# Kernel tuning notes

Measured on AMD Instinct MI355X. Metric: run time of the kernel, lower is better.

## Reference

```python
import jax, jax.numpy as jnp
import numpy as np

TEMP = 0.07
BASE_TEMP = 0.07
LOSS_WEIGHT = 0.5
BN_EPS = 1e-5


def _embed(x, w1, b1, gamma, beta, w2, b2):
    # 1x1 conv C->C  (x: [N,C,H,W], w1: [C_out,C_in])
    h = jnp.einsum('nchw,oc->nohw', x, w1) + b1[None, :, None, None]
    # BatchNorm2d in training mode: batch stats over (N,H,W), biased variance
    mean = h.mean(axis=(0, 2, 3), keepdims=True)
    var = h.var(axis=(0, 2, 3), keepdims=True)
    h = (h - mean) * jax.lax.rsqrt(var + BN_EPS)
    h = h * gamma[None, :, None, None] + beta[None, :, None, None]
    h = jax.nn.relu(h)
    h = jnp.einsum('nchw,oc->nohw', h, w2) + b2[None, :, None, None]
    # F.normalize(p=2, dim=1) with eps=1e-12
    nrm = jnp.sqrt(jnp.sum(h * h, axis=1, keepdims=True))
    return h / jnp.maximum(nrm, 1e-12)


def _contrastive(feats_, labels_):
    # feats_: [T, n_view, C]; labels_: [T]
    T, n_view, C = feats_.shape
    mask_small = (labels_[:, None] == labels_[None, :]).astype(feats_.dtype)  # [T,T]
    # torch.cat(torch.unbind(feats_, dim=1), dim=0): view-major ordering
    cf = feats_.transpose(1, 0, 2).reshape(T * n_view, C)
    logits = (cf @ cf.T) / TEMP                                   # [M,M], M=T*n_view
    logits = logits - jax.lax.stop_gradient(jnp.max(logits, axis=1, keepdims=True))
    mask = jnp.tile(mask_small, (n_view, n_view))                  # repeat(anchor_count, contrast_count)
    neg_mask = 1.0 - mask                                          # computed BEFORE diagonal removal
    M = T * n_view
    logits_mask = 1.0 - jnp.eye(M, dtype=feats_.dtype)
    mask = mask * logits_mask
    exp_logits = jnp.exp(logits)
    neg_logits = jnp.sum(exp_logits * neg_mask, axis=1, keepdims=True)
    log_prob = logits - jnp.log(exp_logits + neg_logits)
    mean_log_prob_pos = jnp.sum(mask * log_prob, axis=1) / (jnp.sum(mask, axis=1) + 1e-6)
    loss = -(TEMP / BASE_TEMP) * mean_log_prob_pos
    return jnp.mean(loss)


def setup_inputs() -> dict:
    N, C_in, H, W = 8, 512, 128, 128
    feat_dim, num_classes = 256, 19
    max_views, max_samples, ignore_label = 100, 1024, -1
    rng = np.random.RandomState(0)

    preds_S = rng.randn(N, C_in, H, W).astype(np.float32)
    # gt label map already at (H,W) => nearest interpolation is identity
    gt = rng.randint(0, num_classes, (N, H * W))
    logits_S = rng.randn(N, num_classes, H * W).astype(np.float32)
    predict = logits_S.argmax(axis=1)  # [N, H*W]

    # ---- replicate _hard_anchor_sampling on host (fixed seed) ----
    classes, total = [], 0
    for i in range(N):
        cl = [int(c) for c in np.unique(gt[i])
              if c != ignore_label and (gt[i] == c).sum() > max_views]
        classes.append(cl)
        total += len(cl)
    n_view = min(max_samples // total, max_views)

    b_idx, p_idx, y_cls = [], [], []
    for i in range(N):
        for c in classes[i]:
            hard = np.where((predict[i] == c) & (gt[i] != c))[0]
            easy = np.where((predict[i] == c) & (gt[i] == c))[0]
            nh, ne = len(hard), len(easy)
            if nh >= n_view / 2 and ne >= n_view / 2:
                kh = n_view // 2; ke = n_view - kh
            elif nh >= n_view / 2:
                ke = ne; kh = n_view - ke
            else:
                kh = nh; ke = n_view - kh
            hs = hard[rng.permutation(nh)[:kh]]
            es = easy[rng.permutation(ne)[:ke]]
            b_idx.append(i)
            p_idx.append(np.concatenate([hs, es]))
            y_cls.append(c)

    batch_idx = jnp.asarray(np.array(b_idx), dtype=jnp.int32)          # [T]
    pix_idx = jnp.asarray(np.stack(p_idx), dtype=jnp.int32)            # [T, n_view]
    y_cls = jnp.asarray(np.array(y_cls), dtype=jnp.int32)              # [T]

    def p(shape, scale, k):
        r = np.random.RandomState(k)
        return jnp.asarray((r.randn(*shape) * scale).astype(np.float32))

    return {
        'preds_S': jnp.asarray(preds_S),
        'w1': p((C_in, C_in), 0.02, 1),
        'b1': jnp.zeros((C_in,), jnp.float32),
        'gamma': jnp.ones((C_in,), jnp.float32),
        'beta': jnp.zeros((C_in,), jnp.float32),
        'w2': p((feat_dim, C_in), 0.02, 2),
        'b2': jnp.zeros((feat_dim,), jnp.float32),
        'batch_idx': batch_idx,
        'pix_idx': pix_idx,
        'y_cls': y_cls,
    }


def reference(preds_S, w1, b1, gamma, beta, w2, b2, batch_idx, pix_idx, y_cls):
    f = _embed(preds_S, w1, b1, gamma, beta, w2, b2)        # [N, C, H, W]
    N, C, H, W = f.shape
    feats = f.transpose(0, 2, 3, 1).reshape(N, H * W, C)     # [N, HW, C]
    X_ = feats[batch_idx[:, None], pix_idx]                   # [T, n_view, C]
    labels_ = y_cls.astype(f.dtype)
    return LOSS_WEIGHT * _contrastive(X_, labels_)
```

## Files before the change

### kernel.cpp

```cpp
#include <hip/hip_runtime.h>
#include <hip/hip_bf16.h>

#define C_IN   512
#define C_OUT  256
#define HW     16384
#define NIMG   8
#define PTOT   (NIMG * HW)
#define MP     1024
#define TEMP_INV (1.0f / 0.07f)
#define BN_EPS   1e-5f
#define SPB    4
#define OGRP   8
#define IGRP   8
#define BK     64

typedef float  f32x4  __attribute__((ext_vector_type(4)));
typedef short  short8 __attribute__((ext_vector_type(8)));
typedef short  short4v __attribute__((ext_vector_type(4)));

#define WS_S1   0
#define WS_G    (WS_S1 + C_IN)
#define WS_W1P  (WS_G + C_IN * C_IN)
#define WS_B1P  (WS_W1P + C_IN * C_IN)
#define WS_CF   (WS_B1P + C_IN)
#define WS_XB_F (WS_CF + MP * C_OUT)
#define WS_NEED_FAST ((size_t)WS_XB_F * 4 + (size_t)PTOT * C_IN * 2)

__global__ __launch_bounds__(256)
void kprep(const float* __restrict__ x, __hip_bfloat16* __restrict__ xb,
           float* __restrict__ s1) {
    int plane = blockIdx.x;
    int c = plane & (C_IN - 1);
    const float4* p = (const float4*)(x + (size_t)plane * HW);
    short4v* q = (short4v*)(xb + (size_t)plane * HW);
    float acc = 0.f;
    for (int i = threadIdx.x; i < HW / 4; i += 256) {
        float4 v = p[i];
        acc += v.x + v.y + v.z + v.w;
        union { short4v s; __hip_bfloat162 h[2]; } u;
        u.h[0] = __float22bfloat162_rn(make_float2(v.x, v.y));
        u.h[1] = __float22bfloat162_rn(make_float2(v.z, v.w));
        q[i] = u.s;
    }
    for (int off = 32; off; off >>= 1) acc += __shfl_down(acc, off, 64);
    __shared__ float red[4];
    int lane = threadIdx.x & 63, wv = threadIdx.x >> 6;
    if (lane == 0) red[wv] = acc;
    __syncthreads();
    if (threadIdx.x == 0)
        atomicAdd(&s1[c], red[0] + red[1] + red[2] + red[3]);
}

__global__ __launch_bounds__(256)
void ksum(const float* __restrict__ x, float* __restrict__ s1) {
    int plane = blockIdx.x;
    int c = plane & (C_IN - 1);
    const float4* p = (const float4*)(x + (size_t)plane * HW);
    float acc = 0.f;
    for (int i = threadIdx.x; i < HW / 4; i += 256) {
        float4 v = p[i];
        acc += v.x + v.y + v.z + v.w;
    }
    for (int off = 32; off; off >>= 1) acc += __shfl_down(acc, off, 64);
    __shared__ float red[4];
    int lane = threadIdx.x & 63, wv = threadIdx.x >> 6;
    if (lane == 0) red[wv] = acc;
    __syncthreads();
    if (threadIdx.x == 0)
        atomicAdd(&s1[c], red[0] + red[1] + red[2] + red[3]);
}

__device__ const int TILE_I[10] = {0,0,0,0,1,1,1,2,2,3};
__device__ const int TILE_J[10] = {0,1,2,3,1,2,3,2,3,3};

__global__ __launch_bounds__(256, 2)
void kgram_bf16(const __hip_bfloat16* __restrict__ xb, float* __restrict__ G) {
    __shared__ __hip_bfloat16 Abuf[2][128 * BK];
    __shared__ __hip_bfloat16 Bbuf[2][128 * BK];
    int tile  = blockIdx.x;
    int chunk = blockIdx.y;
    int n   = chunk >> 4;
    int hw0 = (chunk & 15) * 1024;
    int wave = threadIdx.x >> 6;
    int lane = threadIdx.x & 63;
    int wi = wave >> 1, wj = wave & 1;
    int IT = TILE_I[tile] * 128;
    int JT = TILE_J[tile] * 128;

    const __hip_bfloat16* gA = xb + ((size_t)n * C_IN + IT) * HW + hw0;
    const __hip_bfloat16* gB = xb + ((size_t)n * C_IN + JT) * HW + hw0;

    int rrel = lane >> 3;
    int slot = lane & 7;

    f32x4 acc[4][4];
#pragma unroll
    for (int i = 0; i < 4; ++i)
#pragma unroll
        for (int j = 0; j < 4; ++j) acc[i][j] = {0.f, 0.f, 0.f, 0.f};

    int m  = lane & 15;
    int kq = lane >> 4;

#define STAGE(s, pb)                                                          \
    {                                                                         \
        int kk_ = (s) * BK;                                                   \
        _Pragma("unroll")                                                     \
        for (int i_ = 0; i_ < 4; ++i_) {                                      \
            int row_ = wave * 32 + i_ * 8 + rrel;                             \
            int g_   = slot ^ (row_ & 7);                                     \
            __builtin_amdgcn_global_load_lds(                                 \
                (const __attribute__((address_space(1))) void*)               \
                    (gA + (size_t)row_ * HW + kk_ + g_ * 8),                  \
                (__attribute__((address_space(3))) void*)                     \
                    (&Abuf[pb][(wave * 32 + i_ * 8) * BK]),                   \
                16, 0, 0);                                                    \
            __builtin_amdgcn_global_load_lds(                                 \
                (const __attribute__((address_space(1))) void*)               \
                    (gB + (size_t)row_ * HW + kk_ + g_ * 8),                  \
                (__attribute__((address_space(3))) void*)                     \
                    (&Bbuf[pb][(wave * 32 + i_ * 8) * BK]),                   \
                16, 0, 0);                                                    \
        }                                                                     \
    }

#define COMPUTE(pb)                                                           \
    {                                                                         \
        _Pragma("unroll")                                                     \
        for (int h_ = 0; h_ < 2; ++h_) {                                      \
            short8 af_[4], bf_[4];                                            \
            _Pragma("unroll")                                                 \
            for (int t_ = 0; t_ < 4; ++t_) {                                  \
                int ra_ = wi * 64 + t_ * 16 + m;                              \
                int qa_ = (h_ * 4 + kq) ^ (ra_ & 7);                          \
                af_[t_] = *(const short8*)&Abuf[pb][ra_ * BK + qa_ * 8];      \
                int rb_ = wj * 64 + t_ * 16 + m;                              \
                int qb_ = (h_ * 4 + kq) ^ (rb_ & 7);                          \
                bf_[t_] = *(const short8*)&Bbuf[pb][rb_ * BK + qb_ * 8];      \
            }                                                                 \
            _Pragma("unroll")                                                 \
            for (int i_ = 0; i_ < 4; ++i_)                                    \
                _Pragma("unroll")                                             \
                for (int j_ = 0; j_ < 4; ++j_)                                \
                    acc[i_][j_] = __builtin_amdgcn_mfma_f32_16x16x32_bf16(    \
                        af_[i_], bf_[j_], acc[i_][j_], 0, 0, 0);              \
        }                                                                     \
    }

    STAGE(0, 0)
    __syncthreads();
    int pb = 0;
#pragma unroll 1
    for (int s = 0; s < 16; ++s) {
        if (s < 15) STAGE(s + 1, pb ^ 1)
        COMPUTE(pb)
        __syncthreads();
        pb ^= 1;
    }
#undef STAGE
#undef COMPUTE

    int r0 = (lane >> 4) * 4;
    int cc = lane & 15;
#pragma unroll
    for (int i = 0; i < 4; ++i)
#pragma unroll
        for (int j = 0; j < 4; ++j)
#pragma unroll
            for (int r = 0; r < 4; ++r)
                atomicAdd(&G[(size_t)(IT + wi * 64 + i * 16 + r0 + r) * C_IN
                             + (JT + wj * 64 + j * 16 + cc)],
                          acc[i][j][r]);
}

__global__ __launch_bounds__(256)
void kmirror(float* __restrict__ G) {
    int i = blockIdx.x;
    for (int j = threadIdx.x; j < C_IN; j += 256) {
        if ((i >> 7) > (j >> 7))
            G[(size_t)i * C_IN + j] = G[(size_t)j * C_IN + i];
    }
}

__device__ inline short8 load_frag_f32(const float* p) {
    float4 a = *(const float4*)p;
    float4 b = *(const float4*)(p + 4);
    union { short8 s; __hip_bfloat162 h[4]; } u;
    u.h[0] = __float22bfloat162_rn(make_float2(a.x, a.y));
    u.h[1] = __float22bfloat162_rn(make_float2(a.z, a.w));
    u.h[2] = __float22bfloat162_rn(make_float2(b.x, b.y));
    u.h[3] = __float22bfloat162_rn(make_float2(b.z, b.w));
    return u.s;
}

__global__ __launch_bounds__(256)
void kgram_f32(const float* __restrict__ x, float* __restrict__ G) {
    int bz  = blockIdx.z;
    int n   = bz >> 2;
    int hw0 = (bz & 3) * 4096;
    int wave = threadIdx.x >> 6;
    int lane = threadIdx.x & 63;
    int wi = wave >> 1, wj = wave & 1;
    int I0 = blockIdx.x * 128 + wi * 64;
    int J0 = blockIdx.y * 128 + wj * 64;
    int m    = lane & 15;
    int koff = (lane >> 4) * 8;

    const float* baseA[4];
    const float* baseB[4];
#pragma unroll
    for (int t = 0; t < 4; ++t) {
        baseA[t] = x + ((size_t)n * C_IN + (I0 + t * 16 + m)) * HW + hw0 + koff;
        baseB[t] = x + ((size_t)n * C_IN + (J0 + t * 16 + m)) * HW + hw0 + koff;
    }

    f32x4 acc[4][4];
#pragma unroll
    for (int i = 0; i < 4; ++i)
#pragma unroll
        for (int j = 0; j < 4; ++j) acc[i][j] = {0.f, 0.f, 0.f, 0.f};

    for (int kk = 0; kk < 4096; kk += 32) {
        short8 afr[4], bfr[4];
#pragma unroll
        for (int t = 0; t < 4; ++t) {
            afr[t] = load_frag_f32(baseA[t] + kk);
            bfr[t] = load_frag_f32(baseB[t] + kk);
        }
#pragma unroll
        for (int i = 0; i < 4; ++i)
#pragma unroll
            for (int j = 0; j < 4; ++j)
                acc[i][j] = __builtin_amdgcn_mfma_f32_16x16x32_bf16(
                    afr[i], bfr[j], acc[i][j], 0, 0, 0);
    }

    int r0 = (lane >> 4) * 4;
    int cc = lane & 15;
#pragma unroll
    for (int i = 0; i < 4; ++i)
#pragma unroll
        for (int j = 0; j < 4; ++j)
#pragma unroll
            for (int r = 0; r < 4; ++r)
                atomicAdd(&G[(size_t)(I0 + i * 16 + r0 + r) * C_IN + (J0 + j * 16 + cc)],
                          acc[i][j][r]);
}

__global__ __launch_bounds__(256)
void kstats(const float* __restrict__ w1, const float* __restrict__ b1,
            const float* __restrict__ gamma, const float* __restrict__ beta,
            const float* __restrict__ s1, const float* __restrict__ G,
            float* __restrict__ w1p, float* __restrict__ b1p) {
    int o0 = blockIdx.x * OGRP;
    int tid = threadIdx.x;
    __shared__ float wr[OGRP][C_IN];
    __shared__ float redd[4][OGRP];
    __shared__ float redq[4][OGRP];
    __shared__ float alpha_s[OGRP];

    for (int idx = tid; idx < OGRP * C_IN; idx += 256) {
        int og = idx >> 9, c = idx & (C_IN - 1);
        wr[og][c] = w1[(size_t)(o0 + og) * C_IN + c];
    }
    __syncthreads();

    float dot1[OGRP], quad[OGRP];
#pragma unroll
    for (int og = 0; og < OGRP; ++og) { dot1[og] = 0.f; quad[og] = 0.f; }

    for (int c = tid; c < C_IN; c += 256) {
        const float* gr = G + (size_t)c * C_IN;
        float s1c = s1[c];
        float inner[OGRP];
#pragma unroll
        for (int og = 0; og < OGRP; ++og) inner[og] = 0.f;
        for (int d = 0; d < C_IN; d += 4) {
            float4 gv = *(const float4*)(gr + d);
#pragma unroll
            for (int og = 0; og < OGRP; ++og) {
                float4 wv = *(const float4*)(&wr[og][d]);
                inner[og] += gv.x * wv.x + gv.y * wv.y + gv.z * wv.z + gv.w * wv.w;
            }
        }
#pragma unroll
        for (int og = 0; og < OGRP; ++og) {
            float wc = wr[og][c];
            quad[og] += inner[og] * wc;
            dot1[og] += s1c * wc;
        }
    }
#pragma unroll
    for (int og = 0; og < OGRP; ++og) {
        for (int off = 32; off; off >>= 1) {
            dot1[og] += __shfl_down(dot1[og], off, 64);
            quad[og] += __shfl_down(quad[og], off, 64);
        }
    }
    int lane = tid & 63, wv = tid >> 6;
    if (lane == 0) {
#pragma unroll
        for (int og = 0; og < OGRP; ++og) { redd[wv][og] = dot1[og]; redq[wv][og] = quad[og]; }
    }
    __syncthreads();
    if (tid < OGRP) {
        int og = tid;
        float d1 = redd[0][og] + redd[1][og] + redd[2][og] + redd[3][og];
        float q  = redq[0][og] + redq[1][og] + redq[2][og] + redq[3][og];
        float b  = b1[o0 + og];
        float mean = d1 / (float)PTOT + b;
        float eh2  = (q + 2.f * b * d1) / (float)PTOT + b * b;
        float var  = eh2 - mean * mean;
        float al   = gamma[o0 + og] * rsqrtf(var + BN_EPS);
        alpha_s[og] = al;
        b1p[o0 + og] = beta[o0 + og] + al * (b - mean);
    }
    __syncthreads();
    for (int idx = tid; idx < OGRP * C_IN; idx += 256) {
        int og = idx >> 9, c = idx & (C_IN - 1);
        w1p[(size_t)(o0 + og) * C_IN + c] = alpha_s[og] * wr[og][c];
    }
}

__global__ __launch_bounds__(256)
void kfeat(const float* __restrict__ x, const float* __restrict__ w1p,
           const float* __restrict__ b1p, const float* __restrict__ w2,
           const float* __restrict__ b2, const int* __restrict__ batch_idx,
           const int* __restrict__ pix_idx, float* __restrict__ cf,
           int M, int T, int n_view) {
    __shared__ float xcol[SPB][C_IN];
    __shared__ float h1[SPB][C_IN];
    __shared__ float fl[SPB][C_OUT];
    int tid = threadIdx.x;
    int m0 = blockIdx.x * SPB;

    for (int idx = tid; idx < SPB * C_IN; idx += 256) {
        int s = idx >> 9, c = idx & (C_IN - 1);
        int mm = m0 + s;
        float v = 0.f;
        if (mm < M) {
            int t = mm % T, vv = mm / T;
            int n = batch_idx[t];
            int pix = pix_idx[t * n_view + vv];
            v = x[((size_t)n * C_IN + c) * HW + pix];
        }
        xcol[s][c] = v;
    }
    __syncthreads();

    for (int o = tid; o < C_IN; o += 256) {
        float acc[SPB];
        float bb = b1p[o];
#pragma unroll
        for (int s = 0; s < SPB; ++s) acc[s] = bb;
        const float* wrp = w1p + (size_t)o * C_IN;
        for (int c = 0; c < C_IN; ++c) {
            float w = wrp[c];
#pragma unroll
            for (int s = 0; s < SPB; ++s) acc[s] += w * xcol[s][c];
        }
#pragma unroll
        for (int s = 0; s < SPB; ++s) h1[s][o] = fmaxf(acc[s], 0.f);
    }
    __syncthreads();

    {
        int j = tid;
        float acc[SPB];
        float bb = b2[j];
#pragma unroll
        for (int s = 0; s < SPB; ++s) acc[s] = bb;
        const float* wrp = w2 + (size_t)j * C_IN;
        for (int o = 0; o < C_IN; ++o) {
            float w = wrp[o];
#pragma unroll
            for (int s = 0; s < SPB; ++s) acc[s] += w * h1[s][o];
        }
#pragma unroll
        for (int s = 0; s < SPB; ++s) fl[s][j] = acc[s];
    }
    __syncthreads();

    int wv = tid >> 6, lane = tid & 63;
    {
        float sq = 0.f;
#pragma unroll
        for (int k = 0; k < 4; ++k) { float v = fl[wv][lane + 64 * k]; sq += v * v; }
        for (int off = 32; off; off >>= 1) sq += __shfl_down(sq, off, 64);
        float nrm = __shfl(sq, 0, 64);
        float rinv = 1.f / fmaxf(sqrtf(nrm), 1e-12f);
        int mm = m0 + wv;
        if (mm < M) {
#pragma unroll
            for (int k = 0; k < 4; ++k)
                cf[(size_t)mm * C_OUT + lane + 64 * k] = fl[wv][lane + 64 * k] * rinv;
        }
    }
}

__global__ __launch_bounds__(256)
void kloss(const float* __restrict__ cf, const int* __restrict__ y_cls,
           float* __restrict__ out, int M, int T) {
    int i0 = blockIdx.x * IGRP;
    int tid = threadIdx.x;
    __shared__ float ci[IGRP][C_OUT];
    __shared__ float row[IGRP][MP];
    __shared__ int   lbl[MP];
    __shared__ float redl[IGRP];
    int lane = tid & 63, wv = tid >> 6;

    for (int idx = tid; idx < IGRP * C_OUT; idx += 256) {
        int g = idx >> 8, c = idx & (C_OUT - 1);
        int ii = i0 + g;
        ci[g][c] = (ii < M) ? cf[(size_t)ii * C_OUT + c] : 0.f;
    }
    for (int j = tid; j < M; j += 256) lbl[j] = y_cls[j % T];
    __syncthreads();

    for (int j = tid; j < M; j += 256) {
        const float* cj = cf + (size_t)j * C_OUT;
        float acc[IGRP];
#pragma unroll
        for (int g = 0; g < IGRP; ++g) acc[g] = 0.f;
        for (int c = 0; c < C_OUT; c += 4) {
            float4 v = *(const float4*)(cj + c);
#pragma unroll
            for (int g = 0; g < IGRP; ++g) {
                float4 cv = *(const float4*)(&ci[g][c]);
                acc[g] += cv.x * v.x + cv.y * v.y + cv.z * v.z + cv.w * v.w;
            }
        }
#pragma unroll
        for (int g = 0; g < IGRP; ++g) row[g][j] = acc[g] * TEMP_INV;
    }
    __syncthreads();

    for (int g = wv; g < IGRP; g += 4) {
        int i = i0 + g;
        if (i < M) {
            int lbl_i = lbl[i];
            const float* r = row[g];

            float mx = -1e30f;
            for (int j = lane; j < M; j += 64) mx = fmaxf(mx, r[j]);
            for (int off = 32; off; off >>= 1) mx = fmaxf(mx, __shfl_down(mx, off, 64));
            mx = __shfl(mx, 0, 64);

            float neg = 0.f;
            for (int j = lane; j < M; j += 64)
                if (lbl[j] != lbl_i) neg += expf(r[j] - mx);
            for (int off = 32; off; off >>= 1) neg += __shfl_down(neg, off, 64);
            neg = __shfl(neg, 0, 64);

            float pos = 0.f; int cnt = 0;
            for (int j = lane; j < M; j += 64) {
                if (lbl[j] == lbl_i && j != i) {
                    float l = r[j] - mx;
                    pos += l - logf(expf(l) + neg);
                    cnt++;
                }
            }
            for (int off = 32; off; off >>= 1) {
                pos += __shfl_down(pos, off, 64);
                cnt += __shfl_down(cnt, off, 64);
            }
            if (lane == 0) redl[g] = -pos / ((float)cnt + 1e-6f);
        } else if (lane == 0) redl[g] = 0.f;
    }
    __syncthreads();
    if (tid == 0) {
        float s = 0.f;
        for (int g = 0; g < IGRP; ++g) s += redl[g];
        atomicAdd(out, s * (0.5f / (float)M));
    }
}

extern "C" void kernel_launch(void* const* d_in, const int* in_sizes, int n_in,
                              void* d_out, int out_size, void* d_ws, size_t ws_size,
                              hipStream_t stream) {
    const float* x     = (const float*)d_in[0];
    const float* w1    = (const float*)d_in[1];
    const float* b1    = (const float*)d_in[2];
    const float* gamma = (const float*)d_in[3];
    const float* beta  = (const float*)d_in[4];
    const float* w2    = (const float*)d_in[5];
    const float* b2    = (const float*)d_in[6];
    const int* batch_idx = (const int*)d_in[7];
    const int* pix_idx   = (const int*)d_in[8];
    const int* y_cls     = (const int*)d_in[9];

    int T = in_sizes[7];
    int M = in_sizes[8];
    int n_view = M / T;

    float* ws  = (float*)d_ws;
    float* s1  = ws + WS_S1;
    float* G   = ws + WS_G;
    float* w1p = ws + WS_W1P;
    float* b1p = ws + WS_B1P;
    float* cf  = ws + WS_CF;
    __hip_bfloat16* xb = (__hip_bfloat16*)(ws + WS_XB_F);

    hipMemsetAsync(s1, 0, (size_t)(C_IN + C_IN * C_IN) * sizeof(float), stream);
    hipMemsetAsync(d_out, 0, sizeof(float), stream);

    if (ws_size >= WS_NEED_FAST) {
        kprep<<<NIMG * C_IN, 256, 0, stream>>>(x, xb, s1);
        kgram_bf16<<<dim3(10, 128), 256, 0, stream>>>(xb, G);
        kmirror<<<C_IN, 256, 0, stream>>>(G);
    } else {
        ksum<<<NIMG * C_IN, 256, 0, stream>>>(x, s1);
        kgram_f32<<<dim3(4, 4, 32), 256, 0, stream>>>(x, G);
    }
    kstats<<<C_IN / OGRP, 256, 0, stream>>>(w1, b1, gamma, beta, s1, G, w1p, b1p);
    kfeat<<<(M + SPB - 1) / SPB, 256, 0, stream>>>(x, w1p, b1p, w2, b2,
                                                   batch_idx, pix_idx, cf, M, T, n_view);
    kloss<<<(M + IGRP - 1) / IGRP, 256, 0, stream>>>(cf, y_cls, (float*)d_out, M, T);
}
```

Measured before the change: 706.2 us.

## Single-buffer Gram kernel LDS for higher occupancy; vectorize embedding MLP loads

The bf16 Gram kernel drops its double-buffered LDS staging and raises the launch bound to 4 blocks per CU. It now loads a stage, syncs, computes and syncs again, so latency hiding relies on more resident blocks instead of explicit prefetch overlap. Separately, the two per-sample MLP dot-product loops now read weights and activations as float4 instead of scalars. This cuts load instruction count but changes the summation order slightly.

After: 699.0 us. No clear change (-1.0%).

```diff
diff --git a/kernel.cpp b/kernel.cpp
--- a/kernel.cpp
+++ b/kernel.cpp
@@ -73,10 +73,10 @@
 __device__ const int TILE_I[10] = {0,0,0,0,1,1,1,2,2,3};
 __device__ const int TILE_J[10] = {0,1,2,3,1,2,3,2,3,3};
 
-__global__ __launch_bounds__(256, 2)
+__global__ __launch_bounds__(256, 4)
 void kgram_bf16(const __hip_bfloat16* __restrict__ xb, float* __restrict__ G) {
-    __shared__ __hip_bfloat16 Abuf[2][128 * BK];
-    __shared__ __hip_bfloat16 Bbuf[2][128 * BK];
+    __shared__ __hip_bfloat16 Abuf[128 * BK];
+    __shared__ __hip_bfloat16 Bbuf[128 * BK];
     int tile  = blockIdx.x;
     int chunk = blockIdx.y;
     int n   = chunk >> 4;
@@ -102,63 +102,48 @@
     int m  = lane & 15;
     int kq = lane >> 4;
 
-#define STAGE(s, pb)                                                          \
-    {                                                                         \
-        int kk_ = (s) * BK;                                                   \
-        _Pragma("unroll")                                                     \
-        for (int i_ = 0; i_ < 4; ++i_) {                                      \
-            int row_ = wave * 32 + i_ * 8 + rrel;                             \
-            int g_   = slot ^ (row_ & 7);                                     \
-            __builtin_amdgcn_global_load_lds(                                 \
-                (const __attribute__((address_space(1))) void*)               \
-                    (gA + (size_t)row_ * HW + kk_ + g_ * 8),                  \
-                (__attribute__((address_space(3))) void*)                     \
-                    (&Abuf[pb][(wave * 32 + i_ * 8) * BK]),                   \
-                16, 0, 0);                                                    \
-            __builtin_amdgcn_global_load_lds(                                 \
-                (const __attribute__((address_space(1))) void*)               \
-                    (gB + (size_t)row_ * HW + kk_ + g_ * 8),                  \
-                (__attribute__((address_space(3))) void*)                     \
-                    (&Bbuf[pb][(wave * 32 + i_ * 8) * BK]),                   \
-                16, 0, 0);                                                    \
-        }                                                                     \
-    }
-
-#define COMPUTE(pb)                                                           \
-    {                                                                         \
-        _Pragma("unroll")                                                     \
-        for (int h_ = 0; h_ < 2; ++h_) {                                      \
-            short8 af_[4], bf_[4];                                            \
-            _Pragma("unroll")                                                 \
-            for (int t_ = 0; t_ < 4; ++t_) {                                  \
-                int ra_ = wi * 64 + t_ * 16 + m;                              \
-                int qa_ = (h_ * 4 + kq) ^ (ra_ & 7);                          \
-                af_[t_] = *(const short8*)&Abuf[pb][ra_ * BK + qa_ * 8];      \
-                int rb_ = wj * 64 + t_ * 16 + m;                              \
-                int qb_ = (h_ * 4 + kq) ^ (rb_ & 7);                          \
-                bf_[t_] = *(const short8*)&Bbuf[pb][rb_ * BK + qb_ * 8];      \
-            }                                                                 \
-            _Pragma("unroll")                                                 \
-            for (int i_ = 0; i_ < 4; ++i_)                                    \
-                _Pragma("unroll")                                             \
-                for (int j_ = 0; j_ < 4; ++j_)                                \
-                    acc[i_][j_] = __builtin_amdgcn_mfma_f32_16x16x32_bf16(    \
-                        af_[i_], bf_[j_], acc[i_][j_], 0, 0, 0);              \
-        }                                                                     \
-    }
-
-    STAGE(0, 0)
-    __syncthreads();
-    int pb = 0;
 #pragma unroll 1
     for (int s = 0; s < 16; ++s) {
-        if (s < 15) STAGE(s + 1, pb ^ 1)
-        COMPUTE(pb)
+        int kk = s * BK;
+#pragma unroll
+        for (int i_ = 0; i_ < 4; ++i_) {
+            int row = wave * 32 + i_ * 8 + rrel;
+            int g   = slot ^ (row & 7);
+            __builtin_amdgcn_global_load_lds(
+                (const __attribute__((address_space(1))) void*)
+                    (gA + (size_t)row * HW + kk + g * 8),
+                (__attribute__((address_space(3))) void*)
+                    (&Abuf[(wave * 32 + i_ * 8) * BK]),
+                16, 0, 0);
+            __builtin_amdgcn_global_load_lds(
+                (const __attribute__((address_space(1))) void*)
+                    (gB + (size_t)row * HW + kk + g * 8),
+                (__attribute__((address_space(3))) void*)
+                    (&Bbuf[(wave * 32 + i_ * 8) * BK]),
+                16, 0, 0);
+        }
         __syncthreads();
-        pb ^= 1;
-    }
-#undef STAGE
-#undef COMPUTE
+#pragma unroll
+        for (int h = 0; h < 2; ++h) {
+            short8 af[4], bf[4];
+#pragma unroll
+            for (int t = 0; t < 4; ++t) {
+                int ra = wi * 64 + t * 16 + m;
+                int qa = (h * 4 + kq) ^ (ra & 7);
+                af[t] = *(const short8*)&Abuf[ra * BK + qa * 8];
+                int rb = wj * 64 + t * 16 + m;
+                int qb = (h * 4 + kq) ^ (rb & 7);
+                bf[t] = *(const short8*)&Bbuf[rb * BK + qb * 8];
+            }
+#pragma unroll
+            for (int i_ = 0; i_ < 4; ++i_)
+#pragma unroll
+                for (int j_ = 0; j_ < 4; ++j_)
+                    acc[i_][j_] = __builtin_amdgcn_mfma_f32_16x16x32_bf16(
+                        af[i_], bf[j_], acc[i_][j_], 0, 0, 0);
+        }
+        __syncthreads();
+    }
 
     int r0 = (lane >> 4) * 4;
     int cc = lane & 15;
@@ -354,10 +339,13 @@
 #pragma unroll
         for (int s = 0; s < SPB; ++s) acc[s] = bb;
         const float* wrp = w1p + (size_t)o * C_IN;
-        for (int c = 0; c < C_IN; ++c) {
-            float w = wrp[c];
-#pragma unroll
-            for (int s = 0; s < SPB; ++s) acc[s] += w * xcol[s][c];
+        for (int c = 0; c < C_IN; c += 4) {
+            float4 w = *(const float4*)(wrp + c);
+#pragma unroll
+            for (int s = 0; s < SPB; ++s) {
+                float4 xv = *(const float4*)(&xcol[s][c]);
+                acc[s] += w.x * xv.x + w.y * xv.y + w.z * xv.z + w.w * xv.w;
+            }
         }
 #pragma unroll
         for (int s = 0; s < SPB; ++s) h1[s][o] = fmaxf(acc[s], 0.f);
@@ -371,10 +359,13 @@
 #pragma unroll
         for (int s = 0; s < SPB; ++s) acc[s] = bb;
         const float* wrp = w2 + (size_t)j * C_IN;
-        for (int o = 0; o < C_IN; ++o) {
-            float w = wrp[o];
-#pragma unroll
-            for (int s = 0; s < SPB; ++s) acc[s] += w * h1[s][o];
+        for (int o = 0; o < C_IN; o += 4) {
+            float4 w = *(const float4*)(wrp + o);
+#pragma unroll
+            for (int s = 0; s < SPB; ++s) {
+                float4 hv = *(const float4*)(&h1[s][o]);
+                acc[s] += w.x * hv.x + w.y * hv.y + w.z * hv.z + w.w * hv.w;
+            }
         }
 #pragma unroll
         for (int s = 0; s < SPB; ++s) fl[s][j] = acc[s];
```
